# Optimization experiments

Hardware: AMD Instinct MI355X
Metric: run time of the kernel (lower is better)

The kernel has to match this reference:

```python
import jax, jax.numpy as jnp
import numpy as np

PI = float(np.pi)
N_BINS_POT = 140
TIMESTEP = 0.02
ATOMS = ["N", "CA", "C", "cent"]
ANGLES = [("N", "CA", "C", 0), ("CA", "C", "N", 1), ("C", "N", "CA", 2), ("N", "CA", "cent", 0), ("C", "CA", "cent", 0)]
DIHEDRALS = [("C", "N", "CA", "C", 3), ("N", "CA", "C", "N", 1), ("CA", "C", "N", "CA", 2), ("C", "N", "CA", "cent", 3), ("cent", "CA", "C", "N", 1)]

_gap_ang = (PI - PI / 3) / N_BINS_POT
ANGLE_CENTRES = np.array([PI / 3 + i * _gap_ang + 0.5 * _gap_ang for i in range(N_BINS_POT)][1:-1], dtype=np.float32)  # 138
_gap_dih = 2 * PI / N_BINS_POT
DIH_CENTRES = np.array([-PI + i * _gap_dih - 0.5 * _gap_dih for i in range(N_BINS_POT + 2)][1:-1], dtype=np.float32)  # 140


def safe_norm(v, axis=-1, keepdims=False):
    sq = jnp.sum(v * v, axis=axis, keepdims=keepdims)
    return jnp.where(sq > 0, jnp.sqrt(jnp.where(sq > 0, sq, 1.0)), 0.0)


def normalize(v):
    # torch.nn.functional.normalize with eps=1e-12
    return v / jnp.maximum(safe_norm(v, keepdims=True), 1e-12)


def _gather_force(pots, inds):
    # pots: [n, n_bins]; inds: [b, n] -> 0.5 * (pots[r, i] - pots[r, i+2])
    r = jnp.arange(pots.shape[0])[None, :]
    return 0.5 * (pots[r, inds] - pots[r, inds + 2])


def _accelerations(coords, masses, pair_centres, pair_pots, angle_pots, dih_pots):
    b, n_atoms, _ = coords.shape
    n_res = n_atoms // 4
    # ---- all-pairs distance forces (bin by argmin against per-pair centres, gather) ----
    diffs = coords[:, None, :, :] - coords[:, :, None, :]  # [b, i, j, 3] = c[j] - c[i]
    dists = safe_norm(diffs)  # [b, i, j]
    df = dists.reshape(b, n_atoms * n_atoms)
    inds = jnp.argmin(jnp.abs(pair_centres[None] - df[:, :, None]), axis=2)  # [b, n^2]
    pair_forces = _gather_force(pair_pots, inds).reshape(b, n_atoms, n_atoms)
    norm_diffs = diffs / jnp.maximum(dists, 0.01)[..., None]
    accs = jnp.sum(pair_forces[..., None] * norm_diffs, axis=1) / masses[..., None]
    # ---- bond-angle forces ----
    ac = coords.reshape(b, n_res, 4, 3)
    aa = jnp.zeros_like(ac)
    ang_centres = jnp.asarray(ANGLE_CENTRES)
    for ai, (a1, a2, a3, across) in enumerate(ANGLES):
        i1, i2, i3 = ATOMS.index(a1), ATOMS.index(a2), ATOMS.index(a3)
        if across == 0:
            ba = ac[:, :, i1] - ac[:, :, i2]; bc = ac[:, :, i3] - ac[:, :, i2]; pots = angle_pots[ai]
        elif across == 1:
            ba = ac[:, :-1, i1] - ac[:, :-1, i2]; bc = ac[:, 1:, i3] - ac[:, :-1, i2]; pots = angle_pots[ai][:-1]
        else:
            ba = ac[:, :-1, i1] - ac[:, 1:, i2]; bc = ac[:, 1:, i3] - ac[:, 1:, i2]; pots = angle_pots[ai][1:]
        ban = safe_norm(ba); bcn = safe_norm(bc)
        angs = jnp.arccos(jnp.sum(ba * bc, axis=2) / (ban * bcn))
        ainds = jnp.argmin(jnp.abs(ang_centres[None, None] - angs[:, :, None]), axis=2)
        f = _gather_force(pots, ainds)[..., None]
        cr = jnp.cross(ba, bc)
        fa = f * normalize(jnp.cross(ba, cr)) / ban[..., None]
        fc = f * normalize(jnp.cross(-bc, cr)) / bcn[..., None]
        fb = -fa - fc
        if across == 0:
            aa = aa.at[:, :, i1].add(fa).at[:, :, i2].add(fb).at[:, :, i3].add(fc)
        elif across == 1:
            aa = aa.at[:, :-1, i1].add(fa).at[:, :-1, i2].add(fb).at[:, 1:, i3].add(fc)
        else:
            aa = aa.at[:, :-1, i1].add(fa).at[:, 1:, i2].add(fb).at[:, 1:, i3].add(fc)
    # ---- dihedral forces ----
    dih_centres = jnp.asarray(DIH_CENTRES)
    for di, (a1, a2, a3, a4, across) in enumerate(DIHEDRALS):
        i1, i2, i3, i4 = ATOMS.index(a1), ATOMS.index(a2), ATOMS.index(a3), ATOMS.index(a4)
        if across == 1:
            ab = ac[:, :-1, i2] - ac[:, :-1, i1]; bc = ac[:, :-1, i3] - ac[:, :-1, i2]; cd = ac[:, 1:, i4] - ac[:, :-1, i3]
            pots = dih_pots[di][:-1]
        elif across == 2:
            ab = ac[:, :-1, i2] - ac[:, :-1, i1]; bc = ac[:, 1:, i3] - ac[:, :-1, i2]; cd = ac[:, 1:, i4] - ac[:, 1:, i3]
            pots = dih_pots[di][1:]
        else:  # across == 3
            ab = ac[:, 1:, i2] - ac[:, :-1, i1]; bc = ac[:, 1:, i3] - ac[:, 1:, i2]; cd = ac[:, 1:, i4] - ac[:, 1:, i3]
            pots = dih_pots[di][1:]
        c1 = jnp.cross(ab, bc); c2 = jnp.cross(bc, cd)
        bcn = safe_norm(bc, keepdims=True)
        dihs = jnp.arctan2(jnp.sum(jnp.cross(c1, c2) * bc / bcn, axis=2), jnp.sum(c1 * c2, axis=2))
        dinds = jnp.argmin(jnp.abs(dih_centres[None, None] - dihs[:, :, None]), axis=2)
        f = _gather_force(pots, dinds)[..., None]
        fa = f * normalize(-c1) / safe_norm(ab, keepdims=True)
        fd = f * normalize(c2) / safe_norm(cd, keepdims=True)
        bsq = jnp.squeeze(bcn, -1) ** 2
        t1 = (jnp.sum(ab * bc, axis=2) / bsq)[..., None]
        t2 = (jnp.sum(cd * bc, axis=2) / bsq)[..., None]
        fb = -fa - t1 * fa + t2 * fd  # torque-balancing middle-atom forces
        fc = -fa - fb - fd
        if across == 1:
            aa = aa.at[:, :-1, i1].add(fa).at[:, :-1, i2].add(fb).at[:, :-1, i3].add(fc).at[:, 1:, i4].add(fd)
        elif across == 2:
            aa = aa.at[:, :-1, i1].add(fa).at[:, :-1, i2].add(fb).at[:, 1:, i3].add(fc).at[:, 1:, i4].add(fd)
        else:
            aa = aa.at[:, :-1, i1].add(fa).at[:, 1:, i2].add(fb).at[:, 1:, i3].add(fc).at[:, 1:, i4].add(fd)
    return accs + aa.reshape(b, n_atoms, 3) / masses[..., None]


def _simulate(coords, vels, masses, ff_distances, ff_angles, ff_dihedrals,
              dist_bin_centres, inters_flat, inters_ang, inters_dih, n_steps):
    pair_centres = dist_bin_centres[inters_flat]  # [n^2, 138]
    pair_pots = ff_distances[inters_flat]         # [n^2, 140]
    angle_pots = ff_angles[:, inters_ang]         # [5, n_res, 140]
    dih_pots = ff_dihedrals[:, inters_dih]        # [5, n_res, 142]

    def step(carry, _):
        c, v, a_last = carry
        c = c + v * TIMESTEP + 0.5 * a_last * TIMESTEP * TIMESTEP
        a = _accelerations(c, masses, pair_centres, pair_pots, angle_pots, dih_pots)
        v = v + 0.5 * (a_last + a) * TIMESTEP
        return (c, v, a), None

    (coords, vels, _), _ = jax.lax.scan(step, (coords, vels, jnp.zeros_like(coords)), None, length=n_steps)
    return coords


def setup_inputs() -> dict:
    key = jax.random.key(0)
    ks = jax.random.split(key, 10)
    b, n_res = 1, 100
    n_atoms = n_res * 4
    n2 = n_atoms * n_atoms
    n_dist_types = 4000
    coords = jax.random.normal(ks[0], (b, n_atoms, 3), jnp.float32) * 10.0
    vels = jax.random.normal(ks[1], (b, n_atoms, 3), jnp.float32) * 0.1  # start_temperature = 0.1
    masses = jax.random.uniform(ks[2], (b, n_atoms), jnp.float32, 0.5, 1.5)
    native_coords = jax.random.normal(ks[3], (b, n_atoms, 3), jnp.float32) * 10.0
    ff_distances = jax.random.normal(ks[4], (n_dist_types, 140), jnp.float32) * 0.1
    ff_angles = jax.random.normal(ks[5], (5, 20, 140), jnp.float32) * 0.1
    ff_dihedrals = jax.random.normal(ks[6], (5, 20, 142), jnp.float32) * 0.1
    centres = jnp.linspace(1.0, 15.9, 138, dtype=jnp.float32)
    dist_bin_centres = jnp.tile(centres[None, :], (n_dist_types, 1))
    inters_flat = jax.random.randint(ks[7], (n2,), 0, n_dist_types)
    inters_ang = jax.random.randint(ks[8], (n_res,), 0, 20)
    inters_dih = jax.random.randint(ks[9], (n_res,), 0, 20)
    return {"coords": coords, "vels": vels, "masses": masses, "native_coords": native_coords,
            "ff_distances": ff_distances, "ff_angles": ff_angles, "ff_dihedrals": ff_dihedrals,
            "dist_bin_centres": dist_bin_centres, "inters_flat": inters_flat,
            "inters_ang": inters_ang, "inters_dih": inters_dih, "n_steps": 3}


def reference(coords, vels, masses, native_coords, ff_distances, ff_angles, ff_dihedrals,
              dist_bin_centres, inters_flat, inters_ang, inters_dih, n_steps):
    # native_coords is only used for RMSD reporting in the original; it does not affect the dynamics.
    return _simulate(coords, vels, masses, ff_distances, ff_angles, ff_dihedrals,
                     dist_bin_centres, inters_flat, inters_ang, inters_dih, n_steps)
```

## Files before the change

kernel.cpp:

```cpp
#include <hip/hip_runtime.h>
#include <math.h>

#define N_ATOMS 400
#define N_RES   100
#define DT      0.02f
#define PI_D    3.14159265358979323846

struct V3 { float x, y, z; };
__device__ __forceinline__ V3 v3(float x, float y, float z) { V3 r{x,y,z}; return r; }
__device__ __forceinline__ V3 sub(V3 a, V3 b) { return v3(a.x-b.x, a.y-b.y, a.z-b.z); }
__device__ __forceinline__ V3 neg(V3 a) { return v3(-a.x, -a.y, -a.z); }
__device__ __forceinline__ V3 scale(V3 a, float s) { return v3(a.x*s, a.y*s, a.z*s); }
__device__ __forceinline__ float dot3(V3 a, V3 b) { return a.x*b.x + a.y*b.y + a.z*b.z; }
__device__ __forceinline__ V3 cross3(V3 a, V3 b) {
    return v3(a.y*b.z - a.z*b.y, a.z*b.x - a.x*b.z, a.x*b.y - a.y*b.x);
}
__device__ __forceinline__ float vnorm(V3 a) {
    float s = dot3(a, a);
    return s > 0.0f ? sqrtf(s) : 0.0f;
}
__device__ __forceinline__ V3 normalize3(V3 a) {
    float n = fmaxf(vnorm(a), 1e-12f);
    return scale(a, 1.0f/n);
}

__device__ __forceinline__ int clampi(int i, int lo, int hi) {
    return i < lo ? lo : (i > hi ? hi : i);
}
__device__ __forceinline__ int bin_dist(float d) {
    const float INV = (float)(137.0/14.9);
    return clampi((int)floorf((d - 1.0f)*INV + 0.5f), 0, 137);
}
__device__ __forceinline__ int bin_ang(float a) {
    const float C0  = (float)(PI_D/3.0 + 1.5*((PI_D - PI_D/3.0)/140.0));
    const float INV = (float)(140.0/(PI_D - PI_D/3.0));
    return clampi((int)floorf((a - C0)*INV + 0.5f), 0, 137);
}
__device__ __forceinline__ int bin_dih(float a) {
    const float C0  = (float)(-PI_D + 0.5*(2.0*PI_D/140.0));
    const float INV = (float)(140.0/(2.0*PI_D));
    return clampi((int)floorf((a - C0)*INV + 0.5f), 0, 139);
}

__constant__ int ANG_I[5][3]   = {{0,1,2},{1,2,0},{2,0,1},{0,1,3},{2,1,3}};
__constant__ int ANG_ACROSS[5] = {0,1,2,0,0};
__constant__ int DIH_I[5][4]   = {{2,0,1,2},{0,1,2,0},{1,2,0,1},{2,0,1,3},{3,1,2,0}};
__constant__ int DIH_ACROSS[5] = {3,1,2,3,1};

__device__ __forceinline__ V3 ldpos(const float* c, int res, int atom) {
    int b = (res*4 + atom)*3;
    return v3(c[b], c[b+1], c[b+2]);
}
__device__ __forceinline__ void addF(float* F, int res, int atom, V3 f) {
    int b = (res*4 + atom)*3;
    atomicAdd(&F[b],   f.x);
    atomicAdd(&F[b+1], f.y);
    atomicAdd(&F[b+2], f.z);
}

__global__ void init_kernel(const float* __restrict__ c_in, const float* __restrict__ v_in,
                            float* __restrict__ c, float* __restrict__ v, float* __restrict__ al) {
    int t = blockIdx.x*blockDim.x + threadIdx.x;
    if (t < N_ATOMS*3) { c[t] = c_in[t]; v[t] = v_in[t]; al[t] = 0.0f; }
}

__global__ void pos_kernel(float* __restrict__ c, const float* __restrict__ v,
                           const float* __restrict__ al, float* __restrict__ out) {
    int t = blockIdx.x*blockDim.x + threadIdx.x;
    if (t < N_ATOMS*3) {
        float cc = c[t] + v[t]*DT + 0.5f*al[t]*DT*DT;
        c[t] = cc;
        if (out) out[t] = cc;
    }
}

__global__ void pair_kernel(const float* __restrict__ c, const int* __restrict__ iflat,
                            const float* __restrict__ ffd, float* __restrict__ F) {
    int j = blockIdx.x;
    float cx = c[3*j], cy = c[3*j+1], cz = c[3*j+2];
    float fx = 0.0f, fy = 0.0f, fz = 0.0f;
    for (int i = threadIdx.x; i < N_ATOMS; i += 64) {
        float dx = cx - c[3*i];
        float dy = cy - c[3*i+1];
        float dz = cz - c[3*i+2];
        float d2 = dx*dx + dy*dy + dz*dz;
        float d  = d2 > 0.0f ? sqrtf(d2) : 0.0f;
        int ind  = bin_dist(d);
        int type = iflat[i*N_ATOMS + j];
        const float* row = ffd + (long)type*140;
        float f = 0.5f*(row[ind] - row[ind+2]);
        float w = f / fmaxf(d, 0.01f);
        fx += w*dx; fy += w*dy; fz += w*dz;
    }
    #pragma unroll
    for (int off = 32; off > 0; off >>= 1) {
        fx += __shfl_down(fx, off);
        fy += __shfl_down(fy, off);
        fz += __shfl_down(fz, off);
    }
    if (threadIdx.x == 0) { F[3*j] = fx; F[3*j+1] = fy; F[3*j+2] = fz; }
}

__global__ void bonded_kernel(const float* __restrict__ c, const float* __restrict__ ffa,
                              const float* __restrict__ ffdih, const int* __restrict__ ia,
                              const int* __restrict__ idh, float* __restrict__ F) {
    int t = blockIdx.x*blockDim.x + threadIdx.x;
    if (t < 500) {
        int ai = t/100, r = t%100;
        int across = ANG_ACROSS[ai];
        if (across != 0 && r >= N_RES-1) return;
        int i1 = ANG_I[ai][0], i2 = ANG_I[ai][1], i3 = ANG_I[ai][2];
        int o2 = (across == 2) ? 1 : 0;
        int o3 = (across != 0) ? 1 : 0;
        V3 p1 = ldpos(c, r,     i1);
        V3 p2 = ldpos(c, r+o2,  i2);
        V3 p3 = ldpos(c, r+o3,  i3);
        V3 ba = sub(p1, p2);
        V3 bc = sub(p3, p2);
        float ban = vnorm(ba), bcn = vnorm(bc);
        float ca = dot3(ba, bc) / (ban*bcn);
        ca = fminf(1.0f, fmaxf(-1.0f, ca));
        float ang = acosf(ca);
        int ind = bin_ang(ang);
        int potr = (across == 2) ? r+1 : r;
        const float* row = ffa + (ai*20 + ia[potr])*140;
        float f = 0.5f*(row[ind] - row[ind+2]);
        V3 cr = cross3(ba, bc);
        V3 fa = scale(normalize3(cross3(ba, cr)), f/ban);
        V3 fc = scale(normalize3(neg(cross3(bc, cr))), f/bcn);
        V3 fb = neg(v3(fa.x+fc.x, fa.y+fc.y, fa.z+fc.z));
        addF(F, r,     i1, fa);
        addF(F, r+o2,  i2, fb);
        addF(F, r+o3,  i3, fc);
    } else if (t < 500 + 5*(N_RES-1)) {
        int u = t - 500;
        int di = u/(N_RES-1), r = u%(N_RES-1);
        int across = DIH_ACROSS[di];
        int i1 = DIH_I[di][0], i2 = DIH_I[di][1], i3 = DIH_I[di][2], i4 = DIH_I[di][3];
        int o2 = (across == 3) ? 1 : 0;
        int o3 = (across >= 2) ? 1 : 0;
        int o4 = 1;
        V3 p1 = ldpos(c, r,     i1);
        V3 p2 = ldpos(c, r+o2,  i2);
        V3 p3 = ldpos(c, r+o3,  i3);
        V3 p4 = ldpos(c, r+o4,  i4);
        V3 ab = sub(p2, p1);
        V3 bc = sub(p3, p2);
        V3 cd = sub(p4, p3);
        V3 c1 = cross3(ab, bc);
        V3 c2 = cross3(bc, cd);
        float bcn = vnorm(bc);
        V3 cc = cross3(c1, c2);
        float y = dot3(cc, bc) / bcn;
        float x = dot3(c1, c2);
        float dih = atan2f(y, x);
        int ind = bin_dih(dih);
        int potr = (across == 1) ? r : r+1;
        const float* row = ffdih + (di*20 + idh[potr])*142;
        float f = 0.5f*(row[ind] - row[ind+2]);
        V3 fa = scale(normalize3(neg(c1)), f / vnorm(ab));
        V3 fd = scale(normalize3(c2),      f / vnorm(cd));
        float bsq = bcn*bcn;
        float t1 = dot3(ab, bc)/bsq;
        float t2 = dot3(cd, bc)/bsq;
        V3 fb = v3(-fa.x - t1*fa.x + t2*fd.x,
                   -fa.y - t1*fa.y + t2*fd.y,
                   -fa.z - t1*fa.z + t2*fd.z);
        V3 fc = v3(-fa.x - fb.x - fd.x,
                   -fa.y - fb.y - fd.y,
                   -fa.z - fb.z - fd.z);
        addF(F, r,     i1, fa);
        addF(F, r+o2,  i2, fb);
        addF(F, r+o3,  i3, fc);
        addF(F, r+o4,  i4, fd);
    }
}

__global__ void vel_kernel(const float* __restrict__ F, const float* __restrict__ masses,
                           float* __restrict__ v, float* __restrict__ al) {
    int t = blockIdx.x*blockDim.x + threadIdx.x;
    if (t < N_ATOMS*3) {
        int atom = t/3;
        float a = F[t] / masses[atom];
        v[t] += 0.5f*(al[t] + a)*DT;
        al[t] = a;
    }
}

extern "C" void kernel_launch(void* const* d_in, const int* in_sizes, int n_in,
                              void* d_out, int out_size, void* d_ws, size_t ws_size,
                              hipStream_t stream) {
    const float* coords = (const float*)d_in[0];
    const float* vels   = (const float*)d_in[1];
    const float* masses = (const float*)d_in[2];
    const float* ffd    = (const float*)d_in[4];
    const float* ffa    = (const float*)d_in[5];
    const float* ffdih  = (const float*)d_in[6];
    const int* iflat    = (const int*)d_in[8];
    const int* ia       = (const int*)d_in[9];
    const int* idh      = (const int*)d_in[10];
    float* out = (float*)d_out;

    float* ws = (float*)d_ws;
    float* c  = ws;
    float* v  = ws + 1200;
    float* al = ws + 2400;
    float* F  = ws + 3600;

    init_kernel<<<5, 256, 0, stream>>>(coords, vels, c, v, al);
    const int N_STEPS = 3;
    for (int s = 0; s < N_STEPS; ++s) {
        pos_kernel<<<5, 256, 0, stream>>>(c, v, al, (s == N_STEPS-1) ? out : nullptr);
        if (s < N_STEPS-1) {
            pair_kernel<<<N_ATOMS, 64, 0, stream>>>(c, iflat, ffd, F);
            bonded_kernel<<<4, 256, 0, stream>>>(c, ffa, ffdih, ia, idh, F);
            vel_kernel<<<5, 256, 0, stream>>>(F, masses, v, al);
        }
    }
}
```

Before: 111.7 us.

## Fuse MD step kernels into two force launches plus a closed-form finish

Replaces the per-step chain of init/pos/pair/bonded/vel launches (11 launches) with three: each force kernel recomputes positions on the fly from initial coords, velocities and previous forces, runs pair forces in 100 blocks and bonded forces in one extra block using shared-memory atomics, and a finish kernel applies the closed-form velocity-Verlet update. This targets launch overhead and global atomics on a tiny problem. In exchange, positions are recomputed redundantly per pair access and all bonded work is serialized in a single block, which may lengthen the critical path.

Result: slower. 115.7 us (+3.5%).

```diff
diff --git a/kernel.cpp b/kernel.cpp
--- a/kernel.cpp
+++ b/kernel.cpp
@@ -47,143 +47,175 @@
 __constant__ int DIH_I[5][4]   = {{2,0,1,2},{0,1,2,0},{1,2,0,1},{2,0,1,3},{3,1,2,0}};
 __constant__ int DIH_ACROSS[5] = {3,1,2,3,1};
 
-__device__ __forceinline__ V3 ldpos(const float* c, int res, int atom) {
+__device__ __forceinline__ V3 ldposL(const float* c, int res, int atom) {
     int b = (res*4 + atom)*3;
     return v3(c[b], c[b+1], c[b+2]);
 }
-__device__ __forceinline__ void addF(float* F, int res, int atom, V3 f) {
-    int b = (res*4 + atom)*3;
-    atomicAdd(&F[b],   f.x);
-    atomicAdd(&F[b+1], f.y);
-    atomicAdd(&F[b+2], f.z);
-}
-
-__global__ void init_kernel(const float* __restrict__ c_in, const float* __restrict__ v_in,
-                            float* __restrict__ c, float* __restrict__ v, float* __restrict__ al) {
-    int t = blockIdx.x*blockDim.x + threadIdx.x;
-    if (t < N_ATOMS*3) { c[t] = c_in[t]; v[t] = v_in[t]; al[t] = 0.0f; }
-}
-
-__global__ void pos_kernel(float* __restrict__ c, const float* __restrict__ v,
-                           const float* __restrict__ al, float* __restrict__ out) {
+
+template<int STEP>
+__device__ __forceinline__ float posc(int t, const float* __restrict__ c0,
+                                      const float* __restrict__ v0,
+                                      const float* __restrict__ m,
+                                      const float* __restrict__ Fp1,
+                                      const float* __restrict__ Fb1) {
+    float c = c0[t], v = v0[t];
+    if (STEP == 1) return c + v*DT;
+    float a1 = (Fp1[t] + Fb1[t]) / m[t/3];
+    float v1 = v + 0.5f*a1*DT;
+    return c + v*DT + v1*DT + 0.5f*a1*DT*DT;
+}
+
+template<int STEP>
+__device__ __forceinline__ V3 pos3(int atom, const float* c0, const float* v0,
+                                   const float* m, const float* Fp1, const float* Fb1) {
+    return v3(posc<STEP>(3*atom,   c0, v0, m, Fp1, Fb1),
+              posc<STEP>(3*atom+1, c0, v0, m, Fp1, Fb1),
+              posc<STEP>(3*atom+2, c0, v0, m, Fp1, Fb1));
+}
+
+template<int STEP>
+__global__ __launch_bounds__(256)
+void force_kernel(const float* __restrict__ c0, const float* __restrict__ v0,
+                  const float* __restrict__ m,
+                  const float* __restrict__ Fp1, const float* __restrict__ Fb1,
+                  const int* __restrict__ iflat, const float* __restrict__ ffd,
+                  const float* __restrict__ ffa, const float* __restrict__ ffdih,
+                  const int* __restrict__ ia, const int* __restrict__ idh,
+                  float* __restrict__ Fp, float* __restrict__ Fb) {
+    if (blockIdx.x < 100) {
+        int wave = threadIdx.x >> 6;
+        int lane = threadIdx.x & 63;
+        int j = blockIdx.x*4 + wave;
+        V3 cj = pos3<STEP>(j, c0, v0, m, Fp1, Fb1);
+        float fx = 0.0f, fy = 0.0f, fz = 0.0f;
+        #pragma unroll
+        for (int k = 0; k < 7; ++k) {
+            int i = lane + 64*k;
+            if (i < N_ATOMS) {
+                V3 ci = pos3<STEP>(i, c0, v0, m, Fp1, Fb1);
+                float dx = cj.x - ci.x;
+                float dy = cj.y - ci.y;
+                float dz = cj.z - ci.z;
+                float d2 = dx*dx + dy*dy + dz*dz;
+                float d  = d2 > 0.0f ? sqrtf(d2) : 0.0f;
+                int ind  = bin_dist(d);
+                int type = iflat[i*N_ATOMS + j];
+                const float* row = ffd + (long)type*140;
+                float f = 0.5f*(row[ind] - row[ind+2]);
+                float w = f / fmaxf(d, 0.01f);
+                fx += w*dx; fy += w*dy; fz += w*dz;
+            }
+        }
+        #pragma unroll
+        for (int off = 32; off > 0; off >>= 1) {
+            fx += __shfl_down(fx, off);
+            fy += __shfl_down(fy, off);
+            fz += __shfl_down(fz, off);
+        }
+        if (lane == 0) { Fp[3*j] = fx; Fp[3*j+1] = fy; Fp[3*j+2] = fz; }
+    } else {
+        __shared__ float sc[N_ATOMS*3];
+        __shared__ float sF[N_ATOMS*3];
+        int tid = threadIdx.x;
+        for (int t = tid; t < N_ATOMS*3; t += 256) {
+            sc[t] = posc<STEP>(t, c0, v0, m, Fp1, Fb1);
+            sF[t] = 0.0f;
+        }
+        __syncthreads();
+        for (int item = tid; item < 500 + 5*(N_RES-1); item += 256) {
+            if (item < 500) {
+                int ai = item/100, r = item%100;
+                int across = ANG_ACROSS[ai];
+                if (across != 0 && r >= N_RES-1) continue;
+                int i1 = ANG_I[ai][0], i2 = ANG_I[ai][1], i3 = ANG_I[ai][2];
+                int o2 = (across == 2) ? 1 : 0;
+                int o3 = (across != 0) ? 1 : 0;
+                V3 p1 = ldposL(sc, r,     i1);
+                V3 p2 = ldposL(sc, r+o2,  i2);
+                V3 p3 = ldposL(sc, r+o3,  i3);
+                V3 ba = sub(p1, p2);
+                V3 bc = sub(p3, p2);
+                float ban = vnorm(ba), bcn = vnorm(bc);
+                float ca = dot3(ba, bc) / (ban*bcn);
+                ca = fminf(1.0f, fmaxf(-1.0f, ca));
+                float ang = acosf(ca);
+                int ind = bin_ang(ang);
+                int potr = (across == 2) ? r+1 : r;
+                const float* row = ffa + (ai*20 + ia[potr])*140;
+                float f = 0.5f*(row[ind] - row[ind+2]);
+                V3 cr = cross3(ba, bc);
+                V3 fa = scale(normalize3(cross3(ba, cr)), f/ban);
+                V3 fc = scale(normalize3(neg(cross3(bc, cr))), f/bcn);
+                V3 fb = neg(v3(fa.x+fc.x, fa.y+fc.y, fa.z+fc.z));
+                int b1 = ((r)*4 + i1)*3, b2 = ((r+o2)*4 + i2)*3, b3 = ((r+o3)*4 + i3)*3;
+                atomicAdd(&sF[b1], fa.x); atomicAdd(&sF[b1+1], fa.y); atomicAdd(&sF[b1+2], fa.z);
+                atomicAdd(&sF[b2], fb.x); atomicAdd(&sF[b2+1], fb.y); atomicAdd(&sF[b2+2], fb.z);
+                atomicAdd(&sF[b3], fc.x); atomicAdd(&sF[b3+1], fc.y); atomicAdd(&sF[b3+2], fc.z);
+            } else {
+                int u = item - 500;
+                int di = u/(N_RES-1), r = u%(N_RES-1);
+                int across = DIH_ACROSS[di];
+                int i1 = DIH_I[di][0], i2 = DIH_I[di][1], i3 = DIH_I[di][2], i4 = DIH_I[di][3];
+                int o2 = (across == 3) ? 1 : 0;
+                int o3 = (across >= 2) ? 1 : 0;
+                int o4 = 1;
+                V3 p1 = ldposL(sc, r,     i1);
+                V3 p2 = ldposL(sc, r+o2,  i2);
+                V3 p3 = ldposL(sc, r+o3,  i3);
+                V3 p4 = ldposL(sc, r+o4,  i4);
+                V3 ab = sub(p2, p1);
+                V3 bc = sub(p3, p2);
+                V3 cd = sub(p4, p3);
+                V3 c1 = cross3(ab, bc);
+                V3 c2 = cross3(bc, cd);
+                float bcn = vnorm(bc);
+                V3 cc = cross3(c1, c2);
+                float y = dot3(cc, bc) / bcn;
+                float x = dot3(c1, c2);
+                float dih = atan2f(y, x);
+                int ind = bin_dih(dih);
+                int potr = (across == 1) ? r : r+1;
+                const float* row = ffdih + (di*20 + idh[potr])*142;
+                float f = 0.5f*(row[ind] - row[ind+2]);
+                V3 fa = scale(normalize3(neg(c1)), f / vnorm(ab));
+                V3 fd = scale(normalize3(c2),      f / vnorm(cd));
+                float bsq = bcn*bcn;
+                float t1 = dot3(ab, bc)/bsq;
+                float t2 = dot3(cd, bc)/bsq;
+                V3 fb = v3(-fa.x - t1*fa.x + t2*fd.x,
+                           -fa.y - t1*fa.y + t2*fd.y,
+                           -fa.z - t1*fa.z + t2*fd.z);
+                V3 fc = v3(-fa.x - fb.x - fd.x,
+                           -fa.y - fb.y - fd.y,
+                           -fa.z - fb.z - fd.z);
+                int b1 = ((r)*4 + i1)*3, b2 = ((r+o2)*4 + i2)*3;
+                int b3 = ((r+o3)*4 + i3)*3, b4 = ((r+o4)*4 + i4)*3;
+                atomicAdd(&sF[b1], fa.x); atomicAdd(&sF[b1+1], fa.y); atomicAdd(&sF[b1+2], fa.z);
+                atomicAdd(&sF[b2], fb.x); atomicAdd(&sF[b2+1], fb.y); atomicAdd(&sF[b2+2], fb.z);
+                atomicAdd(&sF[b3], fc.x); atomicAdd(&sF[b3+1], fc.y); atomicAdd(&sF[b3+2], fc.z);
+                atomicAdd(&sF[b4], fd.x); atomicAdd(&sF[b4+1], fd.y); atomicAdd(&sF[b4+2], fd.z);
+            }
+        }
+        __syncthreads();
+        for (int t = tid; t < N_ATOMS*3; t += 256) Fb[t] = sF[t];
+    }
+}
+
+__global__ __launch_bounds__(256)
+void finish_kernel(const float* __restrict__ c0, const float* __restrict__ v0,
+                   const float* __restrict__ m,
+                   const float* __restrict__ Fp1, const float* __restrict__ Fb1,
+                   const float* __restrict__ Fp2, const float* __restrict__ Fb2,
+                   float* __restrict__ out) {
     int t = blockIdx.x*blockDim.x + threadIdx.x;
     if (t < N_ATOMS*3) {
-        float cc = c[t] + v[t]*DT + 0.5f*al[t]*DT*DT;
-        c[t] = cc;
-        if (out) out[t] = cc;
-    }
-}
-
-__global__ void pair_kernel(const float* __restrict__ c, const int* __restrict__ iflat,
-                            const float* __restrict__ ffd, float* __restrict__ F) {
-    int j = blockIdx.x;
-    float cx = c[3*j], cy = c[3*j+1], cz = c[3*j+2];
-    float fx = 0.0f, fy = 0.0f, fz = 0.0f;
-    for (int i = threadIdx.x; i < N_ATOMS; i += 64) {
-        float dx = cx - c[3*i];
-        float dy = cy - c[3*i+1];
-        float dz = cz - c[3*i+2];
-        float d2 = dx*dx + dy*dy + dz*dz;
-        float d  = d2 > 0.0f ? sqrtf(d2) : 0.0f;
-        int ind  = bin_dist(d);
-        int type = iflat[i*N_ATOMS + j];
-        const float* row = ffd + (long)type*140;
-        float f = 0.5f*(row[ind] - row[ind+2]);
-        float w = f / fmaxf(d, 0.01f);
-        fx += w*dx; fy += w*dy; fz += w*dz;
-    }
-    #pragma unroll
-    for (int off = 32; off > 0; off >>= 1) {
-        fx += __shfl_down(fx, off);
-        fy += __shfl_down(fy, off);
-        fz += __shfl_down(fz, off);
-    }
-    if (threadIdx.x == 0) { F[3*j] = fx; F[3*j+1] = fy; F[3*j+2] = fz; }
-}
-
-__global__ void bonded_kernel(const float* __restrict__ c, const float* __restrict__ ffa,
-                              const float* __restrict__ ffdih, const int* __restrict__ ia,
-                              const int* __restrict__ idh, float* __restrict__ F) {
-    int t = blockIdx.x*blockDim.x + threadIdx.x;
-    if (t < 500) {
-        int ai = t/100, r = t%100;
-        int across = ANG_ACROSS[ai];
-        if (across != 0 && r >= N_RES-1) return;
-        int i1 = ANG_I[ai][0], i2 = ANG_I[ai][1], i3 = ANG_I[ai][2];
-        int o2 = (across == 2) ? 1 : 0;
-        int o3 = (across != 0) ? 1 : 0;
-        V3 p1 = ldpos(c, r,     i1);
-        V3 p2 = ldpos(c, r+o2,  i2);
-        V3 p3 = ldpos(c, r+o3,  i3);
-        V3 ba = sub(p1, p2);
-        V3 bc = sub(p3, p2);
-        float ban = vnorm(ba), bcn = vnorm(bc);
-        float ca = dot3(ba, bc) / (ban*bcn);
-        ca = fminf(1.0f, fmaxf(-1.0f, ca));
-        float ang = acosf(ca);
-        int ind = bin_ang(ang);
-        int potr = (across == 2) ? r+1 : r;
-        const float* row = ffa + (ai*20 + ia[potr])*140;
-        float f = 0.5f*(row[ind] - row[ind+2]);
-        V3 cr = cross3(ba, bc);
-        V3 fa = scale(normalize3(cross3(ba, cr)), f/ban);
-        V3 fc = scale(normalize3(neg(cross3(bc, cr))), f/bcn);
-        V3 fb = neg(v3(fa.x+fc.x, fa.y+fc.y, fa.z+fc.z));
-        addF(F, r,     i1, fa);
-        addF(F, r+o2,  i2, fb);
-        addF(F, r+o3,  i3, fc);
-    } else if (t < 500 + 5*(N_RES-1)) {
-        int u = t - 500;
-        int di = u/(N_RES-1), r = u%(N_RES-1);
-        int across = DIH_ACROSS[di];
-        int i1 = DIH_I[di][0], i2 = DIH_I[di][1], i3 = DIH_I[di][2], i4 = DIH_I[di][3];
-        int o2 = (across == 3) ? 1 : 0;
-        int o3 = (across >= 2) ? 1 : 0;
-        int o4 = 1;
-        V3 p1 = ldpos(c, r,     i1);
-        V3 p2 = ldpos(c, r+o2,  i2);
-        V3 p3 = ldpos(c, r+o3,  i3);
-        V3 p4 = ldpos(c, r+o4,  i4);
-        V3 ab = sub(p2, p1);
-        V3 bc = sub(p3, p2);
-        V3 cd = sub(p4, p3);
-        V3 c1 = cross3(ab, bc);
-        V3 c2 = cross3(bc, cd);
-        float bcn = vnorm(bc);
-        V3 cc = cross3(c1, c2);
-        float y = dot3(cc, bc) / bcn;
-        float x = dot3(c1, c2);
-        float dih = atan2f(y, x);
-        int ind = bin_dih(dih);
-        int potr = (across == 1) ? r : r+1;
-        const float* row = ffdih + (di*20 + idh[potr])*142;
-        float f = 0.5f*(row[ind] - row[ind+2]);
-        V3 fa = scale(normalize3(neg(c1)), f / vnorm(ab));
-        V3 fd = scale(normalize3(c2),      f / vnorm(cd));
-        float bsq = bcn*bcn;
-        float t1 = dot3(ab, bc)/bsq;
-        float t2 = dot3(cd, bc)/bsq;
-        V3 fb = v3(-fa.x - t1*fa.x + t2*fd.x,
-                   -fa.y - t1*fa.y + t2*fd.y,
-                   -fa.z - t1*fa.z + t2*fd.z);
-        V3 fc = v3(-fa.x - fb.x - fd.x,
-                   -fa.y - fb.y - fd.y,
-                   -fa.z - fb.z - fd.z);
-        addF(F, r,     i1, fa);
-        addF(F, r+o2,  i2, fb);
-        addF(F, r+o3,  i3, fc);
-        addF(F, r+o4,  i4, fd);
-    }
-}
-
-__global__ void vel_kernel(const float* __restrict__ F, const float* __restrict__ masses,
-                           float* __restrict__ v, float* __restrict__ al) {
-    int t = blockIdx.x*blockDim.x + threadIdx.x;
-    if (t < N_ATOMS*3) {
-        int atom = t/3;
-        float a = F[t] / masses[atom];
-        v[t] += 0.5f*(al[t] + a)*DT;
-        al[t] = a;
+        float im = 1.0f / m[t/3];
+        float a1 = (Fp1[t] + Fb1[t]) * im;
+        float v1 = v0[t] + 0.5f*a1*DT;
+        float c2 = c0[t] + v0[t]*DT + v1*DT + 0.5f*a1*DT*DT;
+        float a2 = (Fp2[t] + Fb2[t]) * im;
+        float v2 = v1 + 0.5f*(a1 + a2)*DT;
+        out[t] = c2 + v2*DT + 0.5f*a2*DT*DT;
     }
 }
 
@@ -201,20 +233,15 @@
     const int* idh      = (const int*)d_in[10];
     float* out = (float*)d_out;
 
-    float* ws = (float*)d_ws;
-    float* c  = ws;
-    float* v  = ws + 1200;
-    float* al = ws + 2400;
-    float* F  = ws + 3600;
-
-    init_kernel<<<5, 256, 0, stream>>>(coords, vels, c, v, al);
-    const int N_STEPS = 3;
-    for (int s = 0; s < N_STEPS; ++s) {
-        pos_kernel<<<5, 256, 0, stream>>>(c, v, al, (s == N_STEPS-1) ? out : nullptr);
-        if (s < N_STEPS-1) {
-            pair_kernel<<<N_ATOMS, 64, 0, stream>>>(c, iflat, ffd, F);
-            bonded_kernel<<<4, 256, 0, stream>>>(c, ffa, ffdih, ia, idh, F);
-            vel_kernel<<<5, 256, 0, stream>>>(F, masses, v, al);
-        }
-    }
-}
+    float* ws  = (float*)d_ws;
+    float* Fp1 = ws;
+    float* Fb1 = ws + 1200;
+    float* Fp2 = ws + 2400;
+    float* Fb2 = ws + 3600;
+
+    force_kernel<1><<<101, 256, 0, stream>>>(coords, vels, masses, nullptr, nullptr,
+                                             iflat, ffd, ffa, ffdih, ia, idh, Fp1, Fb1);
+    force_kernel<2><<<101, 256, 0, stream>>>(coords, vels, masses, Fp1, Fb1,
+                                             iflat, ffd, ffa, ffdih, ia, idh, Fp2, Fb2);
+    finish_kernel<<<5, 256, 0, stream>>>(coords, vels, masses, Fp1, Fb1, Fp2, Fb2, out);
+}
```
